# Optimization experiments

Hardware: AMD Instinct MI355X
Metric: run time of the kernel (lower is better)

## Reference

```python
import jax, jax.numpy as jnp
import numpy as np

A = 0.5  # mixing coefficient `a` from __init__
B, S, C = 16, 4096, 512


def setup_inputs() -> dict:
    key = jax.random.key(0)
    k1, k2 = jax.random.split(key)
    predicted = jax.random.normal(k1, (B, S, C), dtype=jnp.float32)
    target = jax.random.randint(k2, (B, S), 0, C, dtype=jnp.int64)
    return {"predicted": predicted, "target": target}


def reference(predicted, target):
    # predicted: [B, S, C] logits, target: [B, S] int class ids.
    b, s, c = predicted.shape
    am = jnp.argmax(predicted, axis=-1)              # [B, S] per-position top-1 class (topk(1)[1])
    lse = jax.nn.logsumexp(predicted, axis=-1)       # [B, S]

    # counts[i, j, v] = #positions s with target[i,s]==j and argmax==v
    bidx = jnp.arange(b)[:, None]
    counts = jnp.zeros((b, c, c), dtype=jnp.int32).at[bidx, target, am].add(1)
    n = counts.sum(axis=-1)                          # [B, C] occurrences of class j in target[i]
    # torch.mode returns the smallest of the most common values; argmax over class value
    # returns the first (smallest) index achieving the max count, matching that tie-break.
    m = jnp.argmax(counts, axis=-1)                  # [B, C] mode label per (i, j)

    # pred_m[i, j, s] = predicted[i, s, m[i, j]]
    pred_m = predicted[jnp.arange(b)[:, None, None],
                       jnp.arange(s)[None, None, :],
                       m[:, :, None]]                # [B, C, S]
    # per-position CE against constant label m: lse - logit[m]
    term = lse[:, None, :] - pred_m                  # [B, C, S]

    maskT = target[:, None, :] == jnp.arange(c)[None, :, None]  # [B, C, S]
    eq_sum = jnp.sum(jnp.where(maskT, term, 0.0), axis=-1)      # [B, C]
    ne_sum = term.sum(axis=-1) - eq_sum                          # [B, C]

    nf = n.astype(predicted.dtype)
    present = n > 0
    eq_loss = eq_sum / jnp.maximum(nf, 1.0)
    ne_mean = ne_sum / jnp.maximum(s - nf, 1.0)
    ne_loss = 1.0 / jnp.where(present & (ne_mean != 0), ne_mean, 1.0)
    val = eq_loss * (1.0 - A) + A * ne_loss          # [B, C]

    keep = present & (val != 0)                      # cipherLoss[cipherLoss != 0]
    total = jnp.where(keep, val, 0.0).sum()
    cnt = jnp.maximum(keep.sum(), 1).astype(predicted.dtype)
    return total / cnt
```

## Files before the change

kernel.cpp:

```cpp
#include <hip/hip_runtime.h>
#include <cstdint>
#include <cstddef>

#define PB 16
#define PS 4096
#define PC 512

typedef float vf4 __attribute__((ext_vector_type(4)));

__global__ __launch_bounds__(256) void k1_rows(const float* __restrict__ pred,
                                               int* __restrict__ am,
                                               float* __restrict__ lse,
                                               float* __restrict__ colsum) {
    const int t = threadIdx.x, w = t >> 6, l = t & 63;
    const int rowBase = blockIdx.x * 16 + w * 4;
    const int b = rowBase >> 12;
    const float* base = pred + (size_t)rowBase * PC + 4 * l;

    vf4 va[4], vb[4];
    #pragma unroll
    for (int r = 0; r < 4; ++r) {
        va[r] = __builtin_nontemporal_load((const vf4*)(base + r * PC));
        vb[r] = __builtin_nontemporal_load((const vf4*)(base + r * PC + 256));
    }

    float mv[4]; int mi[4];
    #pragma unroll
    for (int r = 0; r < 4; ++r) {
        float m = va[r].x; int i0 = 4 * l;
        if (va[r].y > m) { m = va[r].y; i0 = 4 * l + 1; }
        if (va[r].z > m) { m = va[r].z; i0 = 4 * l + 2; }
        if (va[r].w > m) { m = va[r].w; i0 = 4 * l + 3; }
        if (vb[r].x > m) { m = vb[r].x; i0 = 256 + 4 * l; }
        if (vb[r].y > m) { m = vb[r].y; i0 = 256 + 4 * l + 1; }
        if (vb[r].z > m) { m = vb[r].z; i0 = 256 + 4 * l + 2; }
        if (vb[r].w > m) { m = vb[r].w; i0 = 256 + 4 * l + 3; }
        mv[r] = m; mi[r] = i0;
    }

    #pragma unroll
    for (int off = 1; off < 64; off <<= 1) {
        #pragma unroll
        for (int r = 0; r < 4; ++r) {
            float ov = __shfl_xor(mv[r], off, 64);
            int   oi = __shfl_xor(mi[r], off, 64);
            if (ov > mv[r] || (ov == mv[r] && oi < mi[r])) { mv[r] = ov; mi[r] = oi; }
        }
    }

    float ss[4];
    #pragma unroll
    for (int r = 0; r < 4; ++r) {
        ss[r] = __expf(va[r].x - mv[r]) + __expf(va[r].y - mv[r])
              + __expf(va[r].z - mv[r]) + __expf(va[r].w - mv[r])
              + __expf(vb[r].x - mv[r]) + __expf(vb[r].y - mv[r])
              + __expf(vb[r].z - mv[r]) + __expf(vb[r].w - mv[r]);
    }
    #pragma unroll
    for (int off = 1; off < 64; off <<= 1) {
        #pragma unroll
        for (int r = 0; r < 4; ++r) ss[r] += __shfl_xor(ss[r], off, 64);
    }

    float l0 = mv[0] + __logf(ss[0]);
    float l1 = mv[1] + __logf(ss[1]);
    float l2 = mv[2] + __logf(ss[2]);
    float l3 = mv[3] + __logf(ss[3]);

    if (l == 0) {
        *(float4*)(lse + rowBase) = make_float4(l0, l1, l2, l3);
        *(int4*)(am + rowBase) = make_int4(mi[0], mi[1], mi[2], mi[3]);
    }

    float cs0 = va[0].x + va[1].x + va[2].x + va[3].x;
    float cs1 = va[0].y + va[1].y + va[2].y + va[3].y;
    float cs2 = va[0].z + va[1].z + va[2].z + va[3].z;
    float cs3 = va[0].w + va[1].w + va[2].w + va[3].w;
    float cs4 = vb[0].x + vb[1].x + vb[2].x + vb[3].x;
    float cs5 = vb[0].y + vb[1].y + vb[2].y + vb[3].y;
    float cs6 = vb[0].z + vb[1].z + vb[2].z + vb[3].z;
    float cs7 = vb[0].w + vb[1].w + vb[2].w + vb[3].w;

    __shared__ float lds[4][PC];
    lds[w][4 * l + 0] = cs0; lds[w][4 * l + 1] = cs1;
    lds[w][4 * l + 2] = cs2; lds[w][4 * l + 3] = cs3;
    lds[w][256 + 4 * l + 0] = cs4; lds[w][256 + 4 * l + 1] = cs5;
    lds[w][256 + 4 * l + 2] = cs6; lds[w][256 + 4 * l + 3] = cs7;
    __syncthreads();
    for (int c = t; c < PC; c += 256) {
        float s = lds[0][c] + lds[1][c] + lds[2][c] + lds[3][c];
        atomicAdd(&colsum[(b << 9) + c], s);
    }
}

__global__ __launch_bounds__(512) void k_tail(const float* __restrict__ pred,
                                              const int* __restrict__ target,
                                              const int* __restrict__ am,
                                              const float* __restrict__ lse,
                                              const float* __restrict__ colsum,
                                              float* __restrict__ acc,
                                              int* __restrict__ done,
                                              float* __restrict__ out) {
    __shared__ int   tgam[PS];
    __shared__ float ldsLse[PS];
    __shared__ int   sbucket[PS];
    __shared__ int   sc[PC];
    __shared__ int   cur[PC];
    __shared__ float red[8], redv[8], redk[8];

    const int b = blockIdx.x, t = threadIdx.x;
    cur[t] = 0;
    __syncthreads();

    float lacc = 0.0f;
    for (int i = t; i < PS; i += 512) {
        int gi = (b << 12) + i;
        int tg = target[gi];
        int a  = am[gi];
        float lv = lse[gi];
        tgam[i] = tg | (a << 16);
        ldsLse[i] = lv;
        lacc += lv;
        atomicAdd(&cur[tg], 1);
    }
    #pragma unroll
    for (int off = 1; off < 64; off <<= 1) lacc += __shfl_xor(lacc, off, 64);
    if ((t & 63) == 0) red[t >> 6] = lacc;
    __syncthreads();
    float Ls = red[0] + red[1] + red[2] + red[3] + red[4] + red[5] + red[6] + red[7];

    int x = cur[t];
    sc[t] = x;
    __syncthreads();
    for (int off = 1; off < PC; off <<= 1) {
        int v = (t >= off) ? sc[t - off] : 0;
        __syncthreads();
        sc[t] += v;
        __syncthreads();
    }
    int start = sc[t] - x;
    cur[t] = start;
    __syncthreads();
    for (int i = t; i < PS; i += 512) {
        int e = tgam[i];
        int tg = e & 0xFFFF, a = e >> 16;
        int pos = atomicAdd(&cur[tg], 1);
        sbucket[pos] = i | (a << 12);
    }
    __syncthreads();

    int k = x;
    float val = 0.0f; int keep = 0;
    if (k > 0) {
        int bc = 0, bvv = 0;
        for (int i = 0; i < k; ++i) {
            int v = sbucket[start + i] >> 12;
            int c = 0;
            for (int j = 0; j < k; ++j) c += ((sbucket[start + j] >> 12) == v) ? 1 : 0;
            if (c > bc || (c == bc && v < bvv)) { bc = c; bvv = v; }
        }
        int m = bvv;
        float lseSum = 0.0f;
        float ep0 = 0.0f, ep1 = 0.0f;
        const float* pb = pred + (size_t)(b << 12) * PC + m;
        int i = 0;
        for (; i + 1 < k; i += 2) {
            int s0 = sbucket[start + i] & (PS - 1);
            int s1 = sbucket[start + i + 1] & (PS - 1);
            lseSum += ldsLse[s0] + ldsLse[s1];
            ep0 += pb[(size_t)s0 * PC];
            ep1 += pb[(size_t)s1 * PC];
        }
        if (i < k) {
            int s0 = sbucket[start + i] & (PS - 1);
            lseSum += ldsLse[s0];
            ep0 += pb[(size_t)s0 * PC];
        }
        float eq_sum = lseSum - (ep0 + ep1);
        float ne_sum = (Ls - colsum[(b << 9) + m]) - eq_sum;
        float nf = (float)k;
        float eq_loss = eq_sum / fmaxf(nf, 1.0f);
        float ne_mean = ne_sum / fmaxf((float)PS - nf, 1.0f);
        float ne_loss = 1.0f / ((ne_mean != 0.0f) ? ne_mean : 1.0f);
        val = 0.5f * eq_loss + 0.5f * ne_loss;
        keep = (val != 0.0f) ? 1 : 0;
    }

    float vs = keep ? val : 0.0f;
    float ks = (float)keep;
    #pragma unroll
    for (int off = 1; off < 64; off <<= 1) {
        vs += __shfl_xor(vs, off, 64);
        ks += __shfl_xor(ks, off, 64);
    }
    if ((t & 63) == 0) { redv[t >> 6] = vs; redk[t >> 6] = ks; }
    __syncthreads();
    if (t == 0) {
        float sv = 0.0f, sk = 0.0f;
        #pragma unroll
        for (int i2 = 0; i2 < 8; ++i2) { sv += redv[i2]; sk += redk[i2]; }
        atomicAdd(&acc[0], sv);
        atomicAdd(&acc[1], sk);
        __threadfence();
        int d = atomicAdd(done, 1);
        if (d == PB - 1) {
            __threadfence();
            float a0 = atomicAdd(&acc[0], 0.0f);
            float a1 = atomicAdd(&acc[1], 0.0f);
            out[0] = a0 / fmaxf(a1, 1.0f);
        }
    }
}

extern "C" void kernel_launch(void* const* d_in, const int* in_sizes, int n_in,
                              void* d_out, int out_size, void* d_ws, size_t ws_size,
                              hipStream_t stream) {
    const float* pred = (const float*)d_in[0];
    const int* target = (const int*)d_in[1];
    float* out = (float*)d_out;

    char* w = (char*)d_ws;
    int*   am     = (int*)(w + 0);
    float* lse    = (float*)(w + 262144);
    float* colsum = (float*)(w + 524288);
    float* acc    = (float*)(w + 557056);
    int*   done   = (int*)(w + 557064);

    (void)hipMemsetAsync(w + 524288, 0, 32768 + 12, stream);
    k1_rows<<<(PB * PS) / 16, 256, 0, stream>>>(pred, am, lse, colsum);
    k_tail<<<PB, 512, 0, stream>>>(pred, target, am, lse, colsum, acc, done, out);
}
```

Baseline: 223.1 us.

## Widen tail kernel to 1024 threads with vector loads and wave-scan prefix

The tail kernel now runs 1024 threads per batch block. Each thread loads target, argmax and lse as 4-wide vectors in a single pass. The serial LDS Hillis-Steele scan over 512 class counts is replaced by a wavefront shuffle scan plus per-wave offsets, which cuts the number of barriers. The row kernel also switches from nontemporal loads to plain float4 loads. The per-class mode and gather work still uses only 512 threads and is likely the dominant cost, and the target is read as int32 even though the reference uses int64.

New measurement: 218.7 us. About the same (-2.0%).

```diff
diff --git a/kernel.cpp b/kernel.cpp
--- a/kernel.cpp
+++ b/kernel.cpp
@@ -5,8 +5,6 @@
 #define PB 16
 #define PS 4096
 #define PC 512
-
-typedef float vf4 __attribute__((ext_vector_type(4)));
 
 __global__ __launch_bounds__(256) void k1_rows(const float* __restrict__ pred,
                                                int* __restrict__ am,
@@ -17,11 +15,11 @@
     const int b = rowBase >> 12;
     const float* base = pred + (size_t)rowBase * PC + 4 * l;
 
-    vf4 va[4], vb[4];
+    float4 va[4], vb[4];
     #pragma unroll
     for (int r = 0; r < 4; ++r) {
-        va[r] = __builtin_nontemporal_load((const vf4*)(base + r * PC));
-        vb[r] = __builtin_nontemporal_load((const vf4*)(base + r * PC + 256));
+        va[r] = *(const float4*)(base + r * PC);
+        vb[r] = *(const float4*)(base + r * PC + 256);
     }
 
     float mv[4]; int mi[4];
@@ -93,65 +91,81 @@
     }
 }
 
-__global__ __launch_bounds__(512) void k_tail(const float* __restrict__ pred,
-                                              const int* __restrict__ target,
-                                              const int* __restrict__ am,
-                                              const float* __restrict__ lse,
-                                              const float* __restrict__ colsum,
-                                              float* __restrict__ acc,
-                                              int* __restrict__ done,
-                                              float* __restrict__ out) {
-    __shared__ int   tgam[PS];
+__global__ __launch_bounds__(1024) void k_tail(const float* __restrict__ pred,
+                                               const int* __restrict__ target,
+                                               const int* __restrict__ am,
+                                               const float* __restrict__ lse,
+                                               const float* __restrict__ colsum,
+                                               float* __restrict__ acc,
+                                               int* __restrict__ done,
+                                               float* __restrict__ out) {
     __shared__ float ldsLse[PS];
     __shared__ int   sbucket[PS];
-    __shared__ int   sc[PC];
+    __shared__ int   cnt[PC];
+    __shared__ int   offsA[PC];
     __shared__ int   cur[PC];
-    __shared__ float red[8], redv[8], redk[8];
-
-    const int b = blockIdx.x, t = threadIdx.x;
-    cur[t] = 0;
-    __syncthreads();
-
-    float lacc = 0.0f;
-    for (int i = t; i < PS; i += 512) {
-        int gi = (b << 12) + i;
-        int tg = target[gi];
-        int a  = am[gi];
-        float lv = lse[gi];
-        tgam[i] = tg | (a << 16);
-        ldsLse[i] = lv;
-        lacc += lv;
-        atomicAdd(&cur[tg], 1);
-    }
+    __shared__ float redL[16];
+    __shared__ int   redS[8];
+    __shared__ float redv[16], redk[16];
+
+    const int b = blockIdx.x, t = threadIdx.x, w = t >> 6, l = t & 63;
+    if (t < PC) cnt[t] = 0;
+    __syncthreads();
+
+    const int4*   tg4p = (const int4*)(target + (b << 12));
+    const int4*   am4p = (const int4*)(am + (b << 12));
+    const float4* ls4p = (const float4*)(lse + (b << 12));
+    int4 tg4 = tg4p[t];
+    int4 am4 = am4p[t];
+    float4 ls4 = ls4p[t];
+    ((float4*)ldsLse)[t] = ls4;
+    atomicAdd(&cnt[tg4.x], 1);
+    atomicAdd(&cnt[tg4.y], 1);
+    atomicAdd(&cnt[tg4.z], 1);
+    atomicAdd(&cnt[tg4.w], 1);
+    float lacc = ls4.x + ls4.y + ls4.z + ls4.w;
     #pragma unroll
     for (int off = 1; off < 64; off <<= 1) lacc += __shfl_xor(lacc, off, 64);
-    if ((t & 63) == 0) red[t >> 6] = lacc;
-    __syncthreads();
-    float Ls = red[0] + red[1] + red[2] + red[3] + red[4] + red[5] + red[6] + red[7];
-
-    int x = cur[t];
-    sc[t] = x;
-    __syncthreads();
-    for (int off = 1; off < PC; off <<= 1) {
-        int v = (t >= off) ? sc[t - off] : 0;
-        __syncthreads();
-        sc[t] += v;
-        __syncthreads();
-    }
-    int start = sc[t] - x;
-    cur[t] = start;
-    __syncthreads();
-    for (int i = t; i < PS; i += 512) {
-        int e = tgam[i];
-        int tg = e & 0xFFFF, a = e >> 16;
-        int pos = atomicAdd(&cur[tg], 1);
-        sbucket[pos] = i | (a << 12);
-    }
-    __syncthreads();
-
-    int k = x;
+    if (l == 0) redL[w] = lacc;
+    __syncthreads();
+    float Ls = 0.0f;
+    #pragma unroll
+    for (int j = 0; j < 16; ++j) Ls += redL[j];
+
+    int x = 0, incl = 0;
+    if (t < PC) {
+        x = cnt[t];
+        incl = x;
+        #pragma unroll
+        for (int off = 1; off < 64; off <<= 1) {
+            int v = __shfl_up(incl, off, 64);
+            if (l >= off) incl += v;
+        }
+        if (l == 63) redS[w] = incl;
+    }
+    __syncthreads();
+    if (t < PC) {
+        int woff = 0;
+        #pragma unroll
+        for (int j = 0; j < 8; ++j) woff += (j < w) ? redS[j] : 0;
+        int excl = incl + woff - x;
+        offsA[t] = excl;
+        cur[t] = excl;
+    }
+    __syncthreads();
+
+    {
+        int pos;
+        pos = atomicAdd(&cur[tg4.x], 1); sbucket[pos] = (4 * t + 0) | (am4.x << 12);
+        pos = atomicAdd(&cur[tg4.y], 1); sbucket[pos] = (4 * t + 1) | (am4.y << 12);
+        pos = atomicAdd(&cur[tg4.z], 1); sbucket[pos] = (4 * t + 2) | (am4.z << 12);
+        pos = atomicAdd(&cur[tg4.w], 1); sbucket[pos] = (4 * t + 3) | (am4.w << 12);
+    }
+    __syncthreads();
+
     float val = 0.0f; int keep = 0;
-    if (k > 0) {
+    if (t < PC && x > 0) {
+        int k = x, start = offsA[t];
         int bc = 0, bvv = 0;
         for (int i = 0; i < k; ++i) {
             int v = sbucket[start + i] >> 12;
@@ -160,8 +174,7 @@
             if (c > bc || (c == bc && v < bvv)) { bc = c; bvv = v; }
         }
         int m = bvv;
-        float lseSum = 0.0f;
-        float ep0 = 0.0f, ep1 = 0.0f;
+        float lseSum = 0.0f, ep0 = 0.0f, ep1 = 0.0f;
         const float* pb = pred + (size_t)(b << 12) * PC + m;
         int i = 0;
         for (; i + 1 < k; i += 2) {
@@ -193,12 +206,12 @@
         vs += __shfl_xor(vs, off, 64);
         ks += __shfl_xor(ks, off, 64);
     }
-    if ((t & 63) == 0) { redv[t >> 6] = vs; redk[t >> 6] = ks; }
+    if (l == 0) { redv[w] = vs; redk[w] = ks; }
     __syncthreads();
     if (t == 0) {
         float sv = 0.0f, sk = 0.0f;
         #pragma unroll
-        for (int i2 = 0; i2 < 8; ++i2) { sv += redv[i2]; sk += redk[i2]; }
+        for (int j = 0; j < 16; ++j) { sv += redv[j]; sk += redk[j]; }
         atomicAdd(&acc[0], sv);
         atomicAdd(&acc[1], sk);
         __threadfence();
@@ -228,5 +241,5 @@
 
     (void)hipMemsetAsync(w + 524288, 0, 32768 + 12, stream);
     k1_rows<<<(PB * PS) / 16, 256, 0, stream>>>(pred, am, lse, colsum);
-    k_tail<<<PB, 512, 0, stream>>>(pred, target, am, lse, colsum, acc, done, out);
+    k_tail<<<PB, 1024, 0, stream>>>(pred, target, am, lse, colsum, acc, done, out);
 }
```
